# Performance work log

Hardware: AMD Instinct MI355X
Metric: run time of the kernel (lower is better)

## Reference

```python
import jax, jax.numpy as jnp
import numpy as np

B, N, LQ, DK, DV, DD = 2, 16, 512, 64, 64, 128
TEMPERATURE = 8.0  # sqrt(DK)
NEG_INF = -1e9


def setup_inputs() -> dict:
    key = jax.random.key(0)
    ks = jax.random.split(key, 9)
    h2 = 2 * DD  # dc hidden width = d0 + d1
    return {
        "q": jax.random.normal(ks[0], (B, N, LQ, DK), jnp.float32),
        "k": jax.random.normal(ks[1], (B, N, LQ, DK), jnp.float32),
        "v": jax.random.normal(ks[2], (B, N, LQ, DV), jnp.float32),
        "d0": jax.random.normal(ks[3], (B, LQ, DD), jnp.float32),
        "d1": jax.random.normal(ks[4], (B, LQ, DD), jnp.float32),
        "W1": jax.random.normal(ks[5], (h2, h2), jnp.float32) / np.sqrt(h2),
        "b1": jnp.zeros((h2,), jnp.float32),
        "W2": jax.random.normal(ks[6], (h2, 2), jnp.float32) / np.sqrt(h2),
        "b2": jnp.zeros((2,), jnp.float32),
    }


def reference(q, k, v, d0, d1, W1, b1, W2, b2):
    b, n, lq, dk = q.shape
    dd = d0.shape[-1]
    # pairwise features: f[b,i,j] = concat(d0[b,i], d1[b,j])  -> [b,lq,lq,2dd]
    f = jnp.concatenate(
        [
            jnp.broadcast_to(d0[:, :, None, :], (b, lq, lq, dd)),
            jnp.broadcast_to(d1[:, None, :, :], (b, lq, lq, dd)),
        ],
        axis=-1,
    )
    h = jax.nn.relu(jnp.einsum("bijf,fg->bijg", f, W1) + b1)
    logits = jnp.einsum("bijg,gc->bijc", h, W2) + b2  # [b,lq,lq,2]
    # eval-mode gumbel_softmax(hard=True, tau=1, training=False): argmax of logits
    decisions = (jnp.argmax(logits, axis=-1) == 1)[:, None, :, :]  # [b,1,lq,lq]
    attn = jnp.einsum("bnid,bnjd->bnij", q / TEMPERATURE, k)
    attn = jnp.where(decisions, attn, NEG_INF)
    attn = jax.nn.softmax(attn, axis=-1)  # dropout is identity in eval mode
    output = jnp.einsum("bnij,bnjd->bnid", attn, v)
    return output, attn, decisions
```

## Files before the change

### kernel.cpp

```cpp
#include <hip/hip_runtime.h>

#define BB 2
#define NN 16
#define LQ 512
#define DKk 64
#define DVv 64
#define DDd 128
#define H2 256
#define NEG_INF -1e9f
#define CAP 131072

__global__ __launch_bounds__(256) void mlp_stage1(
    const float* __restrict__ d0, const float* __restrict__ d1,
    const float* __restrict__ W1, const float* __restrict__ b1,
    double* __restrict__ U64, double* __restrict__ W64,
    float* __restrict__ U32, float* __restrict__ W32,
    int* __restrict__ count)
{
    __shared__ float drow[2][DDd];
    int gid = blockIdx.x;
    int half = gid >> 9;
    int r0 = (gid & 511) * 2;
    const float* din = half ? d1 : d0;
    int w1off = half ? DDd : 0;
    double* o64 = half ? W64 : U64;
    float* o32 = half ? W32 : U32;
    int t = threadIdx.x;
    if (gid == 0 && t == 0) *count = 0;
    drow[t >> 7][t & 127] = din[(size_t)(r0 + (t >> 7)) * DDd + (t & 127)];
    __syncthreads();
    int g = t;
    double acc[2] = {};
#pragma unroll 2
    for (int f = 0; f < DDd; f += 4) {
        double w0 = (double)W1[(w1off + f + 0) * H2 + g];
        double w1 = (double)W1[(w1off + f + 1) * H2 + g];
        double w2 = (double)W1[(w1off + f + 2) * H2 + g];
        double w3 = (double)W1[(w1off + f + 3) * H2 + g];
#pragma unroll
        for (int r = 0; r < 2; ++r) {
            float4 dr = *(const float4*)&drow[r][f];
            acc[r] = fma((double)dr.x, w0, acc[r]);
            acc[r] = fma((double)dr.y, w1, acc[r]);
            acc[r] = fma((double)dr.z, w2, acc[r]);
            acc[r] = fma((double)dr.w, w3, acc[r]);
        }
    }
    double bb = half ? 0.0 : (double)b1[g];
#pragma unroll
    for (int r = 0; r < 2; ++r) {
        double a = acc[r] + bb;
        o64[(size_t)(r0 + r) * H2 + g] = a;
        o32[(size_t)(r0 + r) * H2 + g] = (float)a;
    }
}

__global__ __launch_bounds__(256, 4) void dec_full(
    const float* __restrict__ U32, const float* __restrict__ W32,
    const float* __restrict__ W2, const float* __restrict__ b2,
    float* __restrict__ dec_out, int* __restrict__ count, int* __restrict__ list)
{
    __shared__ __align__(16) float Us[16][68];
    __shared__ __align__(16) float Ws[32][68];
    __shared__ __align__(16) float gvs[H2];
    __shared__ int lbuf[512];
    __shared__ int lcnt, lbase;
    int bid = blockIdx.x;
    int b  = bid >> 9;
    int i0 = ((bid >> 4) & 31) * 16;
    int j0 = (bid & 15) * 32;
    int t = threadIdx.x;
    gvs[t] = W2[t * 2 + 1] - W2[t * 2];
    if (t == 0) lcnt = 0;
    float bias = b2[1] - b2[0];
    int ti = t >> 4, tj = t & 15;
    float acc0 = 0.f, acc1 = 0.f;
    for (int gc = 0; gc < H2; gc += 64) {
        __syncthreads();
        {
            int ui = t >> 4, gq = t & 15;
            *(float4*)&Us[ui][gq * 4] =
                *(const float4*)(U32 + ((size_t)(b * LQ) + i0 + ui) * H2 + gc + gq * 4);
        }
        {
            int wj = t >> 3, gq = t & 7;
            const float* src = W32 + ((size_t)(b * LQ) + j0 + wj) * H2 + gc;
            *(float4*)&Ws[wj][gq * 4] = *(const float4*)(src + gq * 4);
            *(float4*)&Ws[wj][(gq + 8) * 4] = *(const float4*)(src + (gq + 8) * 4);
        }
        __syncthreads();
        float4 u_c  = *(const float4*)&Us[ti][0];
        float4 gv_c = *(const float4*)&gvs[gc];
        float4 wA_c = *(const float4*)&Ws[tj][0];
        float4 wB_c = *(const float4*)&Ws[tj + 16][0];
#pragma unroll 5
        for (int gg = 0; gg < 60; gg += 4) {
            float4 u_n  = *(const float4*)&Us[ti][gg + 4];
            float4 gv_n = *(const float4*)&gvs[gc + gg + 4];
            float4 wA_n = *(const float4*)&Ws[tj][gg + 4];
            float4 wB_n = *(const float4*)&Ws[tj + 16][gg + 4];
            acc0 = fmaf(fmaxf(u_c.x + wA_c.x, 0.f), gv_c.x, acc0);
            acc1 = fmaf(fmaxf(u_c.x + wB_c.x, 0.f), gv_c.x, acc1);
            acc0 = fmaf(fmaxf(u_c.y + wA_c.y, 0.f), gv_c.y, acc0);
            acc1 = fmaf(fmaxf(u_c.y + wB_c.y, 0.f), gv_c.y, acc1);
            acc0 = fmaf(fmaxf(u_c.z + wA_c.z, 0.f), gv_c.z, acc0);
            acc1 = fmaf(fmaxf(u_c.z + wB_c.z, 0.f), gv_c.z, acc1);
            acc0 = fmaf(fmaxf(u_c.w + wA_c.w, 0.f), gv_c.w, acc0);
            acc1 = fmaf(fmaxf(u_c.w + wB_c.w, 0.f), gv_c.w, acc1);
            u_c = u_n; gv_c = gv_n; wA_c = wA_n; wB_c = wB_n;
        }
        acc0 = fmaf(fmaxf(u_c.x + wA_c.x, 0.f), gv_c.x, acc0);
        acc1 = fmaf(fmaxf(u_c.x + wB_c.x, 0.f), gv_c.x, acc1);
        acc0 = fmaf(fmaxf(u_c.y + wA_c.y, 0.f), gv_c.y, acc0);
        acc1 = fmaf(fmaxf(u_c.y + wB_c.y, 0.f), gv_c.y, acc1);
        acc0 = fmaf(fmaxf(u_c.z + wA_c.z, 0.f), gv_c.z, acc0);
        acc1 = fmaf(fmaxf(u_c.z + wB_c.z, 0.f), gv_c.z, acc1);
        acc0 = fmaf(fmaxf(u_c.w + wA_c.w, 0.f), gv_c.w, acc0);
        acc1 = fmaf(fmaxf(u_c.w + wB_c.w, 0.f), gv_c.w, acc1);
    }
    int row = b * LQ + i0 + ti;
    float gA = acc0 + bias, gB = acc1 + bias;
    int jA = j0 + tj, jB = j0 + tj + 16;
    dec_out[(size_t)row * LQ + jA] = gA > 0.f ? 1.f : 0.f;
    dec_out[(size_t)row * LQ + jB] = gB > 0.f ? 1.f : 0.f;
    if (fabsf(gA) < 2e-2f) { int lx = atomicAdd(&lcnt, 1); lbuf[lx] = (row << 9) | jA; }
    if (fabsf(gB) < 2e-2f) { int lx = atomicAdd(&lcnt, 1); lbuf[lx] = (row << 9) | jB; }
    __syncthreads();
    if (t == 0 && lcnt > 0) lbase = atomicAdd(count, lcnt);
    __syncthreads();
    for (int x = t; x < lcnt; x += 256) {
        int ix = lbase + x;
        if (ix < CAP) list[ix] = lbuf[x];
    }
}

__global__ __launch_bounds__(256) void gap64_kernel(
    const double* __restrict__ U64, const double* __restrict__ W64,
    const float* __restrict__ W2, const float* __restrict__ b2,
    const int* __restrict__ count, const int* __restrict__ list,
    float* __restrict__ dec_out)
{
    int n = *count; if (n > CAP) n = CAP;
    int gw = (blockIdx.x * 256 + threadIdx.x) >> 6;
    int lane = threadIdx.x & 63;
    int nw = (gridDim.x * 256) >> 6;
    for (int idx = gw; idx < n; idx += nw) {
        int pij = list[idx];
        int j = pij & (LQ - 1);
        int row = pij >> 9;
        int b = row >> 9;
        const double* u = U64 + (size_t)row * H2;
        const double* w = W64 + ((size_t)(b * LQ) + j) * H2;
        double acc = 0.0;
        for (int g = lane; g < H2; g += 64) {
            double tv = u[g] + w[g];
            tv = tv > 0.0 ? tv : 0.0;
            acc = fma(tv, (double)W2[g * 2 + 1] - (double)W2[g * 2 + 0], acc);
        }
#pragma unroll
        for (int off = 32; off; off >>= 1) acc += __shfl_xor(acc, off, 64);
        if (lane == 0) {
            acc += (double)b2[1] - (double)b2[0];
            dec_out[(size_t)row * LQ + j] = acc > 0.0 ? 1.f : 0.f;
        }
    }
}

__global__ __launch_bounds__(256) void fused_attn(
    const float* __restrict__ q, const float* __restrict__ k,
    const float* __restrict__ v, const float* __restrict__ dec,
    float* __restrict__ attn, float* __restrict__ out)
{
    __shared__ __align__(16) float smem[10752];
    float* qT = smem;
    float* kT = smem + 2304;
    float* Ps = smem;
    float* Vs = smem + 2112;
    int bid = blockIdx.x;
    int bn = bid >> 4;
    int i0 = (bid & 15) * 32;
    int b = bn >> 4;
    int t = threadIdx.x;

    {
        int qi = t >> 3;
        const float* src = q + ((size_t)bn * LQ + i0 + qi) * DKk;
#pragma unroll
        for (int it = 0; it < 2; ++it) {
            int kkq = (t & 7) + it * 8;
            float4 t4 = *(const float4*)(src + kkq * 4);
            qT[(kkq * 4 + 0) * 36 + qi] = t4.x;
            qT[(kkq * 4 + 1) * 36 + qi] = t4.y;
            qT[(kkq * 4 + 2) * 36 + qi] = t4.z;
            qT[(kkq * 4 + 3) * 36 + qi] = t4.w;
        }
    }
    int tiq = t >> 5;
    int tjq = t & 31;
    float s[4][4][4];

#pragma unroll
    for (int c = 0; c < 4; ++c) {
        __syncthreads();
        {
            int kj = t >> 2;
#pragma unroll
            for (int it = 0; it < 8; ++it) {
                int jj = kj + (it & 1) * 64;
                int kkq = (t & 3) + (it >> 1) * 4;
                float4 t4 = *(const float4*)(k + ((size_t)bn * LQ + c * 128 + jj) * DKk + kkq * 4);
                kT[(kkq * 4 + 0) * 132 + jj] = t4.x;
                kT[(kkq * 4 + 1) * 132 + jj] = t4.y;
                kT[(kkq * 4 + 2) * 132 + jj] = t4.z;
                kT[(kkq * 4 + 3) * 132 + jj] = t4.w;
            }
        }
        __syncthreads();
        float acc[4][4] = {};
#pragma unroll 8
        for (int kk = 0; kk < 64; ++kk) {
            float4 a  = *(const float4*)&qT[kk * 36 + tiq * 4];
            float4 bb = *(const float4*)&kT[kk * 132 + tjq * 4];
            acc[0][0] = fmaf(a.x, bb.x, acc[0][0]); acc[0][1] = fmaf(a.x, bb.y, acc[0][1]);
            acc[0][2] = fmaf(a.x, bb.z, acc[0][2]); acc[0][3] = fmaf(a.x, bb.w, acc[0][3]);
            acc[1][0] = fmaf(a.y, bb.x, acc[1][0]); acc[1][1] = fmaf(a.y, bb.y, acc[1][1]);
            acc[1][2] = fmaf(a.y, bb.z, acc[1][2]); acc[1][3] = fmaf(a.y, bb.w, acc[1][3]);
            acc[2][0] = fmaf(a.z, bb.x, acc[2][0]); acc[2][1] = fmaf(a.z, bb.y, acc[2][1]);
            acc[2][2] = fmaf(a.z, bb.z, acc[2][2]); acc[2][3] = fmaf(a.z, bb.w, acc[2][3]);
            acc[3][0] = fmaf(a.w, bb.x, acc[3][0]); acc[3][1] = fmaf(a.w, bb.y, acc[3][1]);
            acc[3][2] = fmaf(a.w, bb.z, acc[3][2]); acc[3][3] = fmaf(a.w, bb.w, acc[3][3]);
        }
#pragma unroll
        for (int r = 0; r < 4; ++r) {
            float4 m4 = *(const float4*)&dec[((size_t)(b * LQ) + i0 + tiq * 4 + r) * LQ + c * 128 + tjq * 4];
            s[c][r][0] = m4.x != 0.f ? acc[r][0] * 0.125f : NEG_INF;
            s[c][r][1] = m4.y != 0.f ? acc[r][1] * 0.125f : NEG_INF;
            s[c][r][2] = m4.z != 0.f ? acc[r][2] * 0.125f : NEG_INF;
            s[c][r][3] = m4.w != 0.f ? acc[r][3] * 0.125f : NEG_INF;
        }
    }
#pragma unroll
    for (int r = 0; r < 4; ++r) {
        float m = NEG_INF;
#pragma unroll
        for (int c = 0; c < 4; ++c)
#pragma unroll
            for (int cc = 0; cc < 4; ++cc) m = fmaxf(m, s[c][r][cc]);
#pragma unroll
        for (int off = 1; off < 32; off <<= 1) m = fmaxf(m, __shfl_xor(m, off, 32));
        float sum = 0.f;
#pragma unroll
        for (int c = 0; c < 4; ++c)
#pragma unroll
            for (int cc = 0; cc < 4; ++cc) {
                float e = __expf(s[c][r][cc] - m);
                s[c][r][cc] = e; sum += e;
            }
#pragma unroll
        for (int off = 1; off < 32; off <<= 1) sum += __shfl_xor(sum, off, 32);
        float inv = 1.f / sum;
#pragma unroll
        for (int c = 0; c < 4; ++c)
#pragma unroll
            for (int cc = 0; cc < 4; ++cc) s[c][r][cc] *= inv;
    }
#pragma unroll
    for (int c = 0; c < 4; ++c)
#pragma unroll
        for (int r = 0; r < 4; ++r) {
            float4 wv = make_float4(s[c][r][0], s[c][r][1], s[c][r][2], s[c][r][3]);
            *(float4*)&attn[((size_t)bn * LQ + i0 + tiq * 4 + r) * LQ + c * 128 + tjq * 4] = wv;
        }
    int tio = t >> 4;
    int tdo = t & 15;
    float o[2][4] = {};
#pragma unroll
    for (int c8 = 0; c8 < 8; ++c8) {
        __syncthreads();
        if ((tjq >> 4) == (c8 & 1)) {
            int jl4 = tjq & 15;
            int c = c8 >> 1;
#pragma unroll
            for (int r = 0; r < 4; ++r)
#pragma unroll
                for (int cc = 0; cc < 4; ++cc)
                    Ps[(tiq * 4 + r) * 65 + jl4 * 4 + cc] = s[c][r][cc];
        }
        {
            int vj = t >> 2;
#pragma unroll
            for (int it = 0; it < 4; ++it) {
                int dq = (t & 3) + it * 4;
                *(float4*)&Vs[vj * 68 + dq * 4] =
                    *(const float4*)(v + ((size_t)bn * LQ + c8 * 64 + vj) * DVv + dq * 4);
            }
        }
        __syncthreads();
#pragma unroll 8
        for (int jj = 0; jj < 64; ++jj) {
            float p0 = Ps[(tio * 2 + 0) * 65 + jj];
            float p1 = Ps[(tio * 2 + 1) * 65 + jj];
            float4 v4 = *(const float4*)&Vs[jj * 68 + tdo * 4];
            o[0][0] = fmaf(p0, v4.x, o[0][0]); o[0][1] = fmaf(p0, v4.y, o[0][1]);
            o[0][2] = fmaf(p0, v4.z, o[0][2]); o[0][3] = fmaf(p0, v4.w, o[0][3]);
            o[1][0] = fmaf(p1, v4.x, o[1][0]); o[1][1] = fmaf(p1, v4.y, o[1][1]);
            o[1][2] = fmaf(p1, v4.z, o[1][2]); o[1][3] = fmaf(p1, v4.w, o[1][3]);
        }
    }
#pragma unroll
    for (int rr = 0; rr < 2; ++rr)
        *(float4*)&out[((size_t)bn * LQ + i0 + tio * 2 + rr) * DVv + tdo * 4] =
            make_float4(o[rr][0], o[rr][1], o[rr][2], o[rr][3]);
}

extern "C" void kernel_launch(void* const* d_in, const int* in_sizes, int n_in,
                              void* d_out, int out_size, void* d_ws, size_t ws_size,
                              hipStream_t stream)
{
    const float* q  = (const float*)d_in[0];
    const float* k  = (const float*)d_in[1];
    const float* v  = (const float*)d_in[2];
    const float* d0 = (const float*)d_in[3];
    const float* d1 = (const float*)d_in[4];
    const float* W1 = (const float*)d_in[5];
    const float* b1 = (const float*)d_in[6];
    const float* W2 = (const float*)d_in[7];
    const float* b2 = (const float*)d_in[8];

    float* out  = (float*)d_out;
    float* attn = out + (size_t)BB * NN * LQ * DVv;
    float* dec  = attn + (size_t)BB * NN * LQ * LQ;

    char* scratch = (char*)attn;
    double* U64 = (double*)(scratch);
    double* W64 = (double*)(scratch + (2u << 20));
    float*  U32 = (float*) (scratch + (4u << 20));
    float*  W32 = (float*) (scratch + (5u << 20));
    int* count  = (int*)   (scratch + (6u << 20));
    int* list   = (int*)   (scratch + (6u << 20) + 4096);

    mlp_stage1<<<1024, 256, 0, stream>>>(d0, d1, W1, b1, U64, W64, U32, W32, count);
    dec_full<<<1024, 256, 0, stream>>>(U32, W32, W2, b2, dec, count, list);
    gap64_kernel<<<256, 256, 0, stream>>>(U64, W64, W2, b2, count, list, dec);
    fused_attn<<<512, 256, 0, stream>>>(q, k, v, dec, attn, out);
}
```

Baseline: 175.7 us.

## Remap fused attention so each wave owns full score rows

The QK^T stage now gives each wavefront 8 full query rows across all 512 keys. K is staged in 16-wide depth chunks covering every key, instead of 128-key column chunks. Softmax reductions become a single 64-lane shuffle per row with attn written directly, and P is stored transposed in shared memory so the PV loop reads float4 probabilities and scalar V. This aims to cut cross-thread reduction work and the redundant P staging, at the cost of more live registers (64 floats of scores per thread) and different LDS access patterns.

```diff
diff --git a/kernel.cpp b/kernel.cpp
--- a/kernel.cpp
+++ b/kernel.cpp
@@ -166,21 +166,72 @@
     }
 }
 
+#define QK_R(ar, sa, sb)                                   \
+    sa.x = fmaf(ar, b0.x, sa.x); sa.y = fmaf(ar, b0.y, sa.y); \
+    sa.z = fmaf(ar, b0.z, sa.z); sa.w = fmaf(ar, b0.w, sa.w); \
+    sb.x = fmaf(ar, b1.x, sb.x); sb.y = fmaf(ar, b1.y, sb.y); \
+    sb.z = fmaf(ar, b1.z, sb.z); sb.w = fmaf(ar, b1.w, sb.w);
+
+#define SM_ROW(sa, sb, r) {                                                     \
+    size_t dro = ((size_t)(b * LQ) + i0 + ig * 8 + r) * LQ + lane * 4;          \
+    float4 m0 = *(const float4*)&dec[dro];                                      \
+    float4 m1 = *(const float4*)&dec[dro + 256];                                \
+    sa.x = m0.x != 0.f ? sa.x * 0.125f : NEG_INF;                               \
+    sa.y = m0.y != 0.f ? sa.y * 0.125f : NEG_INF;                               \
+    sa.z = m0.z != 0.f ? sa.z * 0.125f : NEG_INF;                               \
+    sa.w = m0.w != 0.f ? sa.w * 0.125f : NEG_INF;                               \
+    sb.x = m1.x != 0.f ? sb.x * 0.125f : NEG_INF;                               \
+    sb.y = m1.y != 0.f ? sb.y * 0.125f : NEG_INF;                               \
+    sb.z = m1.z != 0.f ? sb.z * 0.125f : NEG_INF;                               \
+    sb.w = m1.w != 0.f ? sb.w * 0.125f : NEG_INF;                               \
+    float mx = fmaxf(fmaxf(fmaxf(sa.x, sa.y), fmaxf(sa.z, sa.w)),              \
+                     fmaxf(fmaxf(sb.x, sb.y), fmaxf(sb.z, sb.w)));              \
+    _Pragma("unroll")                                                            \
+    for (int off = 1; off < 64; off <<= 1) mx = fmaxf(mx, __shfl_xor(mx, off, 64)); \
+    sa.x = __expf(sa.x - mx); sa.y = __expf(sa.y - mx);                         \
+    sa.z = __expf(sa.z - mx); sa.w = __expf(sa.w - mx);                         \
+    sb.x = __expf(sb.x - mx); sb.y = __expf(sb.y - mx);                         \
+    sb.z = __expf(sb.z - mx); sb.w = __expf(sb.w - mx);                         \
+    float sm = sa.x + sa.y + sa.z + sa.w + sb.x + sb.y + sb.z + sb.w;           \
+    _Pragma("unroll")                                                            \
+    for (int off = 1; off < 64; off <<= 1) sm += __shfl_xor(sm, off, 64);       \
+    float inv = 1.f / sm;                                                       \
+    sa.x *= inv; sa.y *= inv; sa.z *= inv; sa.w *= inv;                         \
+    sb.x *= inv; sb.y *= inv; sb.z *= inv; sb.w *= inv;                         \
+    size_t aro = ((size_t)bn * LQ + i0 + ig * 8 + r) * LQ + lane * 4;           \
+    *(float4*)&attn[aro] = sa;                                                  \
+    *(float4*)&attn[aro + 256] = sb;                                            \
+}
+
+#define PT_W(s0, s1, s2, s3, s4, s5, s6, s7) do {                               \
+    int jl4 = (lane & 15) * 4;                                                  \
+    *(float4*)&Pt[(jl4 + 0) * 36 + ig * 8    ] = make_float4(s0.x, s1.x, s2.x, s3.x); \
+    *(float4*)&Pt[(jl4 + 0) * 36 + ig * 8 + 4] = make_float4(s4.x, s5.x, s6.x, s7.x); \
+    *(float4*)&Pt[(jl4 + 1) * 36 + ig * 8    ] = make_float4(s0.y, s1.y, s2.y, s3.y); \
+    *(float4*)&Pt[(jl4 + 1) * 36 + ig * 8 + 4] = make_float4(s4.y, s5.y, s6.y, s7.y); \
+    *(float4*)&Pt[(jl4 + 2) * 36 + ig * 8    ] = make_float4(s0.z, s1.z, s2.z, s3.z); \
+    *(float4*)&Pt[(jl4 + 2) * 36 + ig * 8 + 4] = make_float4(s4.z, s5.z, s6.z, s7.z); \
+    *(float4*)&Pt[(jl4 + 3) * 36 + ig * 8    ] = make_float4(s0.w, s1.w, s2.w, s3.w); \
+    *(float4*)&Pt[(jl4 + 3) * 36 + ig * 8 + 4] = make_float4(s4.w, s5.w, s6.w, s7.w); \
+} while (0)
+
 __global__ __launch_bounds__(256) void fused_attn(
     const float* __restrict__ q, const float* __restrict__ k,
     const float* __restrict__ v, const float* __restrict__ dec,
     float* __restrict__ attn, float* __restrict__ out)
 {
-    __shared__ __align__(16) float smem[10752];
+    __shared__ __align__(16) float smem[10560];
     float* qT = smem;
     float* kT = smem + 2304;
-    float* Ps = smem;
-    float* Vs = smem + 2112;
+    float* Pt = smem;
+    float* Vs = smem + 2304;
     int bid = blockIdx.x;
     int bn = bid >> 4;
     int i0 = (bid & 15) * 32;
     int b = bn >> 4;
     int t = threadIdx.x;
+    int ig = t >> 6;
+    int lane = t & 63;
 
     {
         int qi = t >> 3;
@@ -195,96 +246,48 @@
             qT[(kkq * 4 + 3) * 36 + qi] = t4.w;
         }
     }
-    int tiq = t >> 5;
-    int tjq = t & 31;
-    float s[4][4][4];
-
-#pragma unroll
-    for (int c = 0; c < 4; ++c) {
+
+    float4 sA0 = {}, sA1 = {}, sA2 = {}, sA3 = {}, sA4 = {}, sA5 = {}, sA6 = {}, sA7 = {};
+    float4 sB0 = {}, sB1 = {}, sB2 = {}, sB3 = {}, sB4 = {}, sB5 = {}, sB6 = {}, sB7 = {};
+
+    for (int kc = 0; kc < 4; ++kc) {
         __syncthreads();
         {
-            int kj = t >> 2;
+            int qq = t & 3;
+            int jb = t >> 2;
 #pragma unroll
             for (int it = 0; it < 8; ++it) {
-                int jj = kj + (it & 1) * 64;
-                int kkq = (t & 3) + (it >> 1) * 4;
-                float4 t4 = *(const float4*)(k + ((size_t)bn * LQ + c * 128 + jj) * DKk + kkq * 4);
-                kT[(kkq * 4 + 0) * 132 + jj] = t4.x;
-                kT[(kkq * 4 + 1) * 132 + jj] = t4.y;
-                kT[(kkq * 4 + 2) * 132 + jj] = t4.z;
-                kT[(kkq * 4 + 3) * 132 + jj] = t4.w;
+                int j = jb + it * 64;
+                float4 t4 = *(const float4*)(k + ((size_t)bn * LQ + j) * DKk + kc * 16 + qq * 4);
+                kT[(qq * 4 + 0) * 516 + j] = t4.x;
+                kT[(qq * 4 + 1) * 516 + j] = t4.y;
+                kT[(qq * 4 + 2) * 516 + j] = t4.z;
+                kT[(qq * 4 + 3) * 516 + j] = t4.w;
             }
         }
         __syncthreads();
-        float acc[4][4] = {};
-#pragma unroll 8
-        for (int kk = 0; kk < 64; ++kk) {
-            float4 a  = *(const float4*)&qT[kk * 36 + tiq * 4];
-            float4 bb = *(const float4*)&kT[kk * 132 + tjq * 4];
-            acc[0][0] = fmaf(a.x, bb.x, acc[0][0]); acc[0][1] = fmaf(a.x, bb.y, acc[0][1]);
-            acc[0][2] = fmaf(a.x, bb.z, acc[0][2]); acc[0][3] = fmaf(a.x, bb.w, acc[0][3]);
-            acc[1][0] = fmaf(a.y, bb.x, acc[1][0]); acc[1][1] = fmaf(a.y, bb.y, acc[1][1]);
-            acc[1][2] = fmaf(a.y, bb.z, acc[1][2]); acc[1][3] = fmaf(a.y, bb.w, acc[1][3]);
-            acc[2][0] = fmaf(a.z, bb.x, acc[2][0]); acc[2][1] = fmaf(a.z, bb.y, acc[2][1]);
-            acc[2][2] = fmaf(a.z, bb.z, acc[2][2]); acc[2][3] = fmaf(a.z, bb.w, acc[2][3]);
-            acc[3][0] = fmaf(a.w, bb.x, acc[3][0]); acc[3][1] = fmaf(a.w, bb.y, acc[3][1]);
-            acc[3][2] = fmaf(a.w, bb.z, acc[3][2]); acc[3][3] = fmaf(a.w, bb.w, acc[3][3]);
-        }
-#pragma unroll
-        for (int r = 0; r < 4; ++r) {
-            float4 m4 = *(const float4*)&dec[((size_t)(b * LQ) + i0 + tiq * 4 + r) * LQ + c * 128 + tjq * 4];
-            s[c][r][0] = m4.x != 0.f ? acc[r][0] * 0.125f : NEG_INF;
-            s[c][r][1] = m4.y != 0.f ? acc[r][1] * 0.125f : NEG_INF;
-            s[c][r][2] = m4.z != 0.f ? acc[r][2] * 0.125f : NEG_INF;
-            s[c][r][3] = m4.w != 0.f ? acc[r][3] * 0.125f : NEG_INF;
-        }
-    }
-#pragma unroll
-    for (int r = 0; r < 4; ++r) {
-        float m = NEG_INF;
-#pragma unroll
-        for (int c = 0; c < 4; ++c)
-#pragma unroll
-            for (int cc = 0; cc < 4; ++cc) m = fmaxf(m, s[c][r][cc]);
-#pragma unroll
-        for (int off = 1; off < 32; off <<= 1) m = fmaxf(m, __shfl_xor(m, off, 32));
-        float sum = 0.f;
-#pragma unroll
-        for (int c = 0; c < 4; ++c)
-#pragma unroll
-            for (int cc = 0; cc < 4; ++cc) {
-                float e = __expf(s[c][r][cc] - m);
-                s[c][r][cc] = e; sum += e;
-            }
-#pragma unroll
-        for (int off = 1; off < 32; off <<= 1) sum += __shfl_xor(sum, off, 32);
-        float inv = 1.f / sum;
-#pragma unroll
-        for (int c = 0; c < 4; ++c)
-#pragma unroll
-            for (int cc = 0; cc < 4; ++cc) s[c][r][cc] *= inv;
-    }
-#pragma unroll
-    for (int c = 0; c < 4; ++c)
-#pragma unroll
-        for (int r = 0; r < 4; ++r) {
-            float4 wv = make_float4(s[c][r][0], s[c][r][1], s[c][r][2], s[c][r][3]);
-            *(float4*)&attn[((size_t)bn * LQ + i0 + tiq * 4 + r) * LQ + c * 128 + tjq * 4] = wv;
-        }
-    int tio = t >> 4;
-    int tdo = t & 15;
-    float o[2][4] = {};
-#pragma unroll
-    for (int c8 = 0; c8 < 8; ++c8) {
-        __syncthreads();
-        if ((tjq >> 4) == (c8 & 1)) {
-            int jl4 = tjq & 15;
-            int c = c8 >> 1;
-#pragma unroll
-            for (int r = 0; r < 4; ++r)
-#pragma unroll
-                for (int cc = 0; cc < 4; ++cc)
-                    Ps[(tiq * 4 + r) * 65 + jl4 * 4 + cc] = s[c][r][cc];
+#pragma unroll
+        for (int kk = 0; kk < 16; ++kk) {
+            float4 a0 = *(const float4*)&qT[(kc * 16 + kk) * 36 + ig * 8];
+            float4 a1 = *(const float4*)&qT[(kc * 16 + kk) * 36 + ig * 8 + 4];
+            float4 b0 = *(const float4*)&kT[kk * 516 + lane * 4];
+            float4 b1 = *(const float4*)&kT[kk * 516 + 256 + lane * 4];
+            QK_R(a0.x, sA0, sB0); QK_R(a0.y, sA1, sB1);
+            QK_R(a0.z, sA2, sB2); QK_R(a0.w, sA3, sB3);
+            QK_R(a1.x, sA4, sB4); QK_R(a1.y, sA5, sB5);
+            QK_R(a1.z, sA6, sB6); QK_R(a1.w, sA7, sB7);
+        }
+    }
+
+    SM_ROW(sA0, sB0, 0); SM_ROW(sA1, sB1, 1); SM_ROW(sA2, sB2, 2); SM_ROW(sA3, sB3, 3);
+    SM_ROW(sA4, sB4, 4); SM_ROW(sA5, sB5, 5); SM_ROW(sA6, sB6, 6); SM_ROW(sA7, sB7, 7);
+
+    float o[8] = {};
+    for (int c = 0; c < 8; ++c) {
+        __syncthreads();
+        if ((lane >> 4) == (c & 3)) {
+            if (c < 4) { PT_W(sA0, sA1, sA2, sA3, sA4, sA5, sA6, sA7); }
+            else       { PT_W(sB0, sB1, sB2, sB3, sB4, sB5, sB6, sB7); }
         }
         {
             int vj = t >> 2;
@@ -292,25 +295,24 @@
             for (int it = 0; it < 4; ++it) {
                 int dq = (t & 3) + it * 4;
                 *(float4*)&Vs[vj * 68 + dq * 4] =
-                    *(const float4*)(v + ((size_t)bn * LQ + c8 * 64 + vj) * DVv + dq * 4);
+                    *(const float4*)(v + ((size_t)bn * LQ + c * 64 + vj) * DVv + dq * 4);
             }
         }
         __syncthreads();
 #pragma unroll 8
         for (int jj = 0; jj < 64; ++jj) {
-            float p0 = Ps[(tio * 2 + 0) * 65 + jj];
-            float p1 = Ps[(tio * 2 + 1) * 65 + jj];
-            float4 v4 = *(const float4*)&Vs[jj * 68 + tdo * 4];
-            o[0][0] = fmaf(p0, v4.x, o[0][0]); o[0][1] = fmaf(p0, v4.y, o[0][1]);
-            o[0][2] = fmaf(p0, v4.z, o[0][2]); o[0][3] = fmaf(p0, v4.w, o[0][3]);
-            o[1][0] = fmaf(p1, v4.x, o[1][0]); o[1][1] = fmaf(p1, v4.y, o[1][1]);
-            o[1][2] = fmaf(p1, v4.z, o[1][2]); o[1][3] = fmaf(p1, v4.w, o[1][3]);
-        }
-    }
-#pragma unroll
-    for (int rr = 0; rr < 2; ++rr)
-        *(float4*)&out[((size_t)bn * LQ + i0 + tio * 2 + rr) * DVv + tdo * 4] =
-            make_float4(o[rr][0], o[rr][1], o[rr][2], o[rr][3]);
+            float4 pa = *(const float4*)&Pt[jj * 36 + ig * 8];
+            float4 pb = *(const float4*)&Pt[jj * 36 + ig * 8 + 4];
+            float vv = Vs[jj * 68 + lane];
+            o[0] = fmaf(pa.x, vv, o[0]); o[1] = fmaf(pa.y, vv, o[1]);
+            o[2] = fmaf(pa.z, vv, o[2]); o[3] = fmaf(pa.w, vv, o[3]);
+            o[4] = fmaf(pb.x, vv, o[4]); o[5] = fmaf(pb.y, vv, o[5]);
+            o[6] = fmaf(pb.z, vv, o[6]); o[7] = fmaf(pb.w, vv, o[7]);
+        }
+    }
+#pragma unroll
+    for (int r = 0; r < 8; ++r)
+        out[((size_t)bn * LQ + i0 + ig * 8 + r) * DVv + lane] = o[r];
 }
 
 extern "C" void kernel_launch(void* const* d_in, const int* in_sizes, int n_in,
```

After: 181.5 us. 3.3% more time.

## Fuse fp64 near-tie recheck into decision kernel and restructure PV loop

Applied to the files above, without the earlier changes.

The separate gap64 kernel and its global count/list handoff are removed. Each dec_full block now re-evaluates its own near-zero-margin decisions in double precision straight from its shared-memory list, which saves a kernel launch and the global atomics. The P·V stage in fused_attn is also reorganised: P is stored transposed so it can be read with float4 loads, each thread handles 8 rows over a quarter of the j range, and the partial sums are combined with cross-lane shuffles. The trade-off is more registers for the 8x4 accumulator and some serial fp64 tail work inside dec_full blocks.

```diff
diff --git a/kernel.cpp b/kernel.cpp
--- a/kernel.cpp
+++ b/kernel.cpp
@@ -8,14 +8,12 @@
 #define DDd 128
 #define H2 256
 #define NEG_INF -1e9f
-#define CAP 131072
 
 __global__ __launch_bounds__(256) void mlp_stage1(
     const float* __restrict__ d0, const float* __restrict__ d1,
     const float* __restrict__ W1, const float* __restrict__ b1,
     double* __restrict__ U64, double* __restrict__ W64,
-    float* __restrict__ U32, float* __restrict__ W32,
-    int* __restrict__ count)
+    float* __restrict__ U32, float* __restrict__ W32)
 {
     __shared__ float drow[2][DDd];
     int gid = blockIdx.x;
@@ -26,7 +24,6 @@
     double* o64 = half ? W64 : U64;
     float* o32 = half ? W32 : U32;
     int t = threadIdx.x;
-    if (gid == 0 && t == 0) *count = 0;
     drow[t >> 7][t & 127] = din[(size_t)(r0 + (t >> 7)) * DDd + (t & 127)];
     __syncthreads();
     int g = t;
@@ -57,14 +54,15 @@
 
 __global__ __launch_bounds__(256, 4) void dec_full(
     const float* __restrict__ U32, const float* __restrict__ W32,
+    const double* __restrict__ U64, const double* __restrict__ W64,
     const float* __restrict__ W2, const float* __restrict__ b2,
-    float* __restrict__ dec_out, int* __restrict__ count, int* __restrict__ list)
+    float* __restrict__ dec_out)
 {
     __shared__ __align__(16) float Us[16][68];
     __shared__ __align__(16) float Ws[32][68];
     __shared__ __align__(16) float gvs[H2];
     __shared__ int lbuf[512];
-    __shared__ int lcnt, lbase;
+    __shared__ int lcnt;
     int bid = blockIdx.x;
     int b  = bid >> 9;
     int i0 = ((bid >> 4) & 31) * 16;
@@ -126,45 +124,33 @@
     if (fabsf(gA) < 2e-2f) { int lx = atomicAdd(&lcnt, 1); lbuf[lx] = (row << 9) | jA; }
     if (fabsf(gB) < 2e-2f) { int lx = atomicAdd(&lcnt, 1); lbuf[lx] = (row << 9) | jB; }
     __syncthreads();
-    if (t == 0 && lcnt > 0) lbase = atomicAdd(count, lcnt);
-    __syncthreads();
-    for (int x = t; x < lcnt; x += 256) {
-        int ix = lbase + x;
-        if (ix < CAP) list[ix] = lbuf[x];
-    }
-}
-
-__global__ __launch_bounds__(256) void gap64_kernel(
-    const double* __restrict__ U64, const double* __restrict__ W64,
-    const float* __restrict__ W2, const float* __restrict__ b2,
-    const int* __restrict__ count, const int* __restrict__ list,
-    float* __restrict__ dec_out)
-{
-    int n = *count; if (n > CAP) n = CAP;
-    int gw = (blockIdx.x * 256 + threadIdx.x) >> 6;
-    int lane = threadIdx.x & 63;
-    int nw = (gridDim.x * 256) >> 6;
-    for (int idx = gw; idx < n; idx += nw) {
-        int pij = list[idx];
+    int nloc = lcnt;
+    int wv = t >> 6, ln = t & 63;
+    for (int x = wv; x < nloc; x += 4) {
+        int pij = lbuf[x];
         int j = pij & (LQ - 1);
-        int row = pij >> 9;
-        int b = row >> 9;
-        const double* u = U64 + (size_t)row * H2;
-        const double* w = W64 + ((size_t)(b * LQ) + j) * H2;
+        int prow = pij >> 9;
+        int pb = prow >> 9;
+        const double* u = U64 + (size_t)prow * H2;
+        const double* w = W64 + ((size_t)(pb * LQ) + j) * H2;
         double acc = 0.0;
-        for (int g = lane; g < H2; g += 64) {
+        for (int g = ln; g < H2; g += 64) {
             double tv = u[g] + w[g];
             tv = tv > 0.0 ? tv : 0.0;
             acc = fma(tv, (double)W2[g * 2 + 1] - (double)W2[g * 2 + 0], acc);
         }
 #pragma unroll
         for (int off = 32; off; off >>= 1) acc += __shfl_xor(acc, off, 64);
-        if (lane == 0) {
+        if (ln == 0) {
             acc += (double)b2[1] - (double)b2[0];
-            dec_out[(size_t)row * LQ + j] = acc > 0.0 ? 1.f : 0.f;
+            dec_out[(size_t)prow * LQ + j] = acc > 0.0 ? 1.f : 0.f;
         }
     }
 }
+
+#define PV5R(pp, rr)                                                       \
+    o[rr][0] = fmaf(pp, v4.x, o[rr][0]); o[rr][1] = fmaf(pp, v4.y, o[rr][1]); \
+    o[rr][2] = fmaf(pp, v4.z, o[rr][2]); o[rr][3] = fmaf(pp, v4.w, o[rr][3]);
 
 __global__ __launch_bounds__(256) void fused_attn(
     const float* __restrict__ q, const float* __restrict__ k,
@@ -174,8 +160,8 @@
     __shared__ __align__(16) float smem[10752];
     float* qT = smem;
     float* kT = smem + 2304;
-    float* Ps = smem;
-    float* Vs = smem + 2112;
+    float* Pt = smem;
+    float* Vs = smem + 2304;
     int bid = blockIdx.x;
     int bn = bid >> 4;
     int i0 = (bid & 15) * 32;
@@ -271,46 +257,60 @@
             float4 wv = make_float4(s[c][r][0], s[c][r][1], s[c][r][2], s[c][r][3]);
             *(float4*)&attn[((size_t)bn * LQ + i0 + tiq * 4 + r) * LQ + c * 128 + tjq * 4] = wv;
         }
-    int tio = t >> 4;
-    int tdo = t & 15;
-    float o[2][4] = {};
+
+    int oct = t >> 6;
+    int lane = t & 63;
+    int jq = lane >> 4;
+    int dq = lane & 15;
+    float o[8][4] = {};
 #pragma unroll
     for (int c8 = 0; c8 < 8; ++c8) {
         __syncthreads();
         if ((tjq >> 4) == (c8 & 1)) {
-            int jl4 = tjq & 15;
+            int jl = tjq & 15;
             int c = c8 >> 1;
-#pragma unroll
-            for (int r = 0; r < 4; ++r)
-#pragma unroll
-                for (int cc = 0; cc < 4; ++cc)
-                    Ps[(tiq * 4 + r) * 65 + jl4 * 4 + cc] = s[c][r][cc];
+            *(float4*)&Pt[(jl * 4 + 0) * 36 + tiq * 4] =
+                make_float4(s[c][0][0], s[c][1][0], s[c][2][0], s[c][3][0]);
+            *(float4*)&Pt[(jl * 4 + 1) * 36 + tiq * 4] =
+                make_float4(s[c][0][1], s[c][1][1], s[c][2][1], s[c][3][1]);
+            *(float4*)&Pt[(jl * 4 + 2) * 36 + tiq * 4] =
+                make_float4(s[c][0][2], s[c][1][2], s[c][2][2], s[c][3][2]);
+            *(float4*)&Pt[(jl * 4 + 3) * 36 + tiq * 4] =
+                make_float4(s[c][0][3], s[c][1][3], s[c][2][3], s[c][3][3]);
         }
         {
             int vj = t >> 2;
 #pragma unroll
             for (int it = 0; it < 4; ++it) {
-                int dq = (t & 3) + it * 4;
-                *(float4*)&Vs[vj * 68 + dq * 4] =
-                    *(const float4*)(v + ((size_t)bn * LQ + c8 * 64 + vj) * DVv + dq * 4);
+                int dqs = (t & 3) + it * 4;
+                *(float4*)&Vs[vj * 72 + dqs * 4] =
+                    *(const float4*)(v + ((size_t)bn * LQ + c8 * 64 + vj) * DVv + dqs * 4);
             }
         }
         __syncthreads();
-#pragma unroll 8
-        for (int jj = 0; jj < 64; ++jj) {
-            float p0 = Ps[(tio * 2 + 0) * 65 + jj];
-            float p1 = Ps[(tio * 2 + 1) * 65 + jj];
-            float4 v4 = *(const float4*)&Vs[jj * 68 + tdo * 4];
-            o[0][0] = fmaf(p0, v4.x, o[0][0]); o[0][1] = fmaf(p0, v4.y, o[0][1]);
-            o[0][2] = fmaf(p0, v4.z, o[0][2]); o[0][3] = fmaf(p0, v4.w, o[0][3]);
-            o[1][0] = fmaf(p1, v4.x, o[1][0]); o[1][1] = fmaf(p1, v4.y, o[1][1]);
-            o[1][2] = fmaf(p1, v4.z, o[1][2]); o[1][3] = fmaf(p1, v4.w, o[1][3]);
-        }
-    }
-#pragma unroll
-    for (int rr = 0; rr < 2; ++rr)
-        *(float4*)&out[((size_t)bn * LQ + i0 + tio * 2 + rr) * DVv + tdo * 4] =
-            make_float4(o[rr][0], o[rr][1], o[rr][2], o[rr][3]);
+#pragma unroll
+        for (int s16 = 0; s16 < 16; ++s16) {
+            int jj = jq * 16 + s16;
+            float4 v4 = *(const float4*)&Vs[jj * 72 + dq * 4];
+            float4 pl = *(const float4*)&Pt[jj * 36 + oct * 8];
+            float4 ph = *(const float4*)&Pt[jj * 36 + oct * 8 + 4];
+            PV5R(pl.x, 0) PV5R(pl.y, 1) PV5R(pl.z, 2) PV5R(pl.w, 3)
+            PV5R(ph.x, 4) PV5R(ph.y, 5) PV5R(ph.z, 6) PV5R(ph.w, 7)
+        }
+    }
+#pragma unroll
+    for (int r = 0; r < 8; ++r)
+#pragma unroll
+        for (int d = 0; d < 4; ++d) {
+            o[r][d] += __shfl_xor(o[r][d], 16, 64);
+            o[r][d] += __shfl_xor(o[r][d], 32, 64);
+        }
+    if (jq == 0) {
+#pragma unroll
+        for (int r = 0; r < 8; ++r)
+            *(float4*)&out[((size_t)bn * LQ + i0 + oct * 8 + r) * DVv + dq * 4] =
+                make_float4(o[r][0], o[r][1], o[r][2], o[r][3]);
+    }
 }
 
 extern "C" void kernel_launch(void* const* d_in, const int* in_sizes, int n_in,
@@ -336,11 +336,8 @@
     double* W64 = (double*)(scratch + (2u << 20));
     float*  U32 = (float*) (scratch + (4u << 20));
     float*  W32 = (float*) (scratch + (5u << 20));
-    int* count  = (int*)   (scratch + (6u << 20));
-    int* list   = (int*)   (scratch + (6u << 20) + 4096);
-
-    mlp_stage1<<<1024, 256, 0, stream>>>(d0, d1, W1, b1, U64, W64, U32, W32, count);
-    dec_full<<<1024, 256, 0, stream>>>(U32, W32, W2, b2, dec, count, list);
-    gap64_kernel<<<256, 256, 0, stream>>>(U64, W64, W2, b2, count, list, dec);
+
+    mlp_stage1<<<1024, 256, 0, stream>>>(d0, d1, W1, b1, U64, W64, U32, W32);
+    dec_full<<<1024, 256, 0, stream>>>(U32, W32, U64, W64, W2, b2, dec);
     fused_attn<<<512, 256, 0, stream>>>(q, k, v, dec, attn, out);
 }
```

Result: no change. 178.1 us (+1.4%).
